# Performance work log

Measured on AMD Instinct MI355X. Metric: run time of the kernel, lower is better.

Reference implementation:

```python
import jax, jax.numpy as jnp
import numpy as np

B, N = 8192, 2048
_EPS = 1e-5


def setup_inputs() -> dict:
    key = jax.random.key(0)
    k1, k2, k3 = jax.random.split(key, 3)
    src = jax.random.normal(k1, (B, 3, N), dtype=jnp.float32)
    src_corr = jax.random.normal(k2, (B, 3, N), dtype=jnp.float32)
    weights = jax.random.uniform(k3, (B, N), dtype=jnp.float32)
    return {"src": src, "src_corr": src_corr, "weights": weights}


def reference(src, src_corr, weights):
    # src, src_corr: (B, 3, N); weights: (B, N)
    a = jnp.swapaxes(src, -1, -2)        # (B, N, 3)
    b = jnp.swapaxes(src_corr, -1, -2)   # (B, N, 3)
    w = weights[..., None]               # (B, N, 1)
    wn = w / (jnp.sum(w, axis=1, keepdims=True) + _EPS)
    centroid_a = jnp.sum(a * wn, axis=1)  # (B, 3)
    centroid_b = jnp.sum(b * wn, axis=1)  # (B, 3)
    a_c = a - centroid_a[:, None, :]
    b_c = b - centroid_b[:, None, :]
    # cov = a_c^T @ (b_c * wn) -> (B, 3, 3)
    cov = jnp.einsum('bnd,bne->bde', a_c, b_c * wn)
    u, s, vh = jnp.linalg.svd(cov, full_matrices=False)
    v = jnp.swapaxes(vh, -1, -2)
    ut = jnp.swapaxes(u, -1, -2)
    rot_pos = v @ ut
    v_neg = v.at[:, :, 2].multiply(-1.0)  # flip last column of v
    rot_neg = v_neg @ ut
    rot = jnp.where(jnp.linalg.det(rot_pos)[:, None, None] > 0, rot_pos, rot_neg)
    translation = centroid_b - jnp.einsum('bij,bj->bi', rot, centroid_a)  # (B, 3)
    return rot, translation
```

## Files before the change

kernel.cpp:

```cpp
#include <hip/hip_runtime.h>
#include <math.h>


constexpr int kB = 8192;
constexpr int kN = 2048;
constexpr float kEps = 1e-5f;

__global__ __launch_bounds__(256) void wproc_kernel(
    const float* __restrict__ src,
    const float* __restrict__ src_corr,
    const float* __restrict__ weights,
    float* __restrict__ out)
{
    const int b = blockIdx.x;
    const float* wrow = weights + (size_t)b * kN;
    const float* arow = src + (size_t)b * 3 * kN;
    const float* brow = src_corr + (size_t)b * 3 * kN;

    float acc[16];
#pragma unroll
    for (int i = 0; i < 16; ++i) acc[i] = 0.f;

    const float4* w4  = reinterpret_cast<const float4*>(wrow);
    const float4* ax4 = reinterpret_cast<const float4*>(arow);
    const float4* ay4 = reinterpret_cast<const float4*>(arow + kN);
    const float4* az4 = reinterpret_cast<const float4*>(arow + 2 * kN);
    const float4* bx4 = reinterpret_cast<const float4*>(brow);
    const float4* by4 = reinterpret_cast<const float4*>(brow + kN);
    const float4* bz4 = reinterpret_cast<const float4*>(brow + 2 * kN);

    for (int i = threadIdx.x; i < kN / 4; i += blockDim.x) {
        float4 w  = w4[i];
        float4 ax = ax4[i], ay = ay4[i], az = az4[i];
        float4 bx = bx4[i], by = by4[i], bz = bz4[i];
        float wc[4]  = {w.x,  w.y,  w.z,  w.w};
        float axc[4] = {ax.x, ax.y, ax.z, ax.w};
        float ayc[4] = {ay.x, ay.y, ay.z, ay.w};
        float azc[4] = {az.x, az.y, az.z, az.w};
        float bxc[4] = {bx.x, bx.y, bx.z, bx.w};
        float byc[4] = {by.x, by.y, by.z, by.w};
        float bzc[4] = {bz.x, bz.y, bz.z, bz.w};
#pragma unroll
        for (int c = 0; c < 4; ++c) {
            float ww  = wc[c];
            float wax = ww * axc[c], way = ww * ayc[c], waz = ww * azc[c];
            float bxx = bxc[c], byy = byc[c], bzz = bzc[c];
            acc[0]  += ww;
            acc[1]  += wax;       acc[2]  += way;       acc[3]  += waz;
            acc[4]  += ww * bxx;  acc[5]  += ww * byy;  acc[6]  += ww * bzz;
            acc[7]  += wax * bxx; acc[8]  += wax * byy; acc[9]  += wax * bzz;
            acc[10] += way * bxx; acc[11] += way * byy; acc[12] += way * bzz;
            acc[13] += waz * bxx; acc[14] += waz * byy; acc[15] += waz * bzz;
        }
    }

#pragma unroll
    for (int i = 0; i < 16; ++i) {
        float v = acc[i];
        for (int off = 32; off > 0; off >>= 1)
            v += __shfl_down(v, off, 64);
        acc[i] = v;
    }

    __shared__ float red[4][16];
    const int lane = threadIdx.x & 63;
    const int wid  = threadIdx.x >> 6;
    if (lane == 0) {
#pragma unroll
        for (int i = 0; i < 16; ++i) red[wid][i] = acc[i];
    }
    __syncthreads();
    if (threadIdx.x != 0) return;

    float t[16];
#pragma unroll
    for (int i = 0; i < 16; ++i)
        t[i] = red[0][i] + red[1][i] + red[2][i] + red[3][i];

    const float W   = t[0];
    const float inv = 1.f / (W + kEps);
    const float S   = W * inv;
    float ca[3], cb[3];
#pragma unroll
    for (int d = 0; d < 3; ++d) { ca[d] = t[1 + d] * inv; cb[d] = t[4 + d] * inv; }

    float M[3][3];
    const float f2 = 2.f - S;
#pragma unroll
    for (int d = 0; d < 3; ++d)
#pragma unroll
        for (int e = 0; e < 3; ++e)
            M[d][e] = t[7 + 3 * d + e] * inv - ca[d] * cb[e] * f2;

    const float T  = M[0][0] + M[1][1] + M[2][2];
    const float cx = M[1][2] - M[2][1];
    const float cy = M[2][0] - M[0][2];
    const float cz = M[0][1] - M[1][0];
    float Nm[4][4];
    Nm[0][0] = T;
    Nm[0][1] = Nm[1][0] = cx;
    Nm[0][2] = Nm[2][0] = cy;
    Nm[0][3] = Nm[3][0] = cz;
    Nm[1][1] = 2.f * M[0][0] - T;
    Nm[2][2] = 2.f * M[1][1] - T;
    Nm[3][3] = 2.f * M[2][2] - T;
    Nm[1][2] = Nm[2][1] = M[0][1] + M[1][0];
    Nm[1][3] = Nm[3][1] = M[0][2] + M[2][0];
    Nm[2][3] = Nm[3][2] = M[1][2] + M[2][1];

    float Vv[4][4] = {{1,0,0,0},{0,1,0,0},{0,0,1,0},{0,0,0,1}};
    const int pp[6] = {0,0,0,1,1,2};
    const int qq[6] = {1,2,3,2,3,3};
    for (int sweep = 0; sweep < 6; ++sweep) {
        for (int r = 0; r < 6; ++r) {
            const int p = pp[r], q = qq[r];
            const float apq = Nm[p][q];
            if (fabsf(apq) < 1e-12f) continue;
            const float tau = (Nm[q][q] - Nm[p][p]) / (2.f * apq);
            const float tt  = copysignf(1.f, tau) / (fabsf(tau) + sqrtf(1.f + tau * tau));
            const float c   = 1.f / sqrtf(1.f + tt * tt);
            const float s   = tt * c;
            const float app = Nm[p][p], aqq = Nm[q][q];
            Nm[p][p] = app - tt * apq;
            Nm[q][q] = aqq + tt * apq;
            Nm[p][q] = Nm[q][p] = 0.f;
#pragma unroll
            for (int k = 0; k < 4; ++k) {
                if (k == p || k == q) continue;
                const float akp = Nm[k][p], akq = Nm[k][q];
                Nm[k][p] = Nm[p][k] = c * akp - s * akq;
                Nm[k][q] = Nm[q][k] = s * akp + c * akq;
            }
#pragma unroll
            for (int k = 0; k < 4; ++k) {
                const float vkp = Vv[k][p], vkq = Vv[k][q];
                Vv[k][p] = c * vkp - s * vkq;
                Vv[k][q] = s * vkp + c * vkq;
            }
        }
    }

    int jm = 0;
    for (int j = 1; j < 4; ++j) if (Nm[j][j] > Nm[jm][jm]) jm = j;
    float qw = Vv[0][jm], qx = Vv[1][jm], qy = Vv[2][jm], qz = Vv[3][jm];
    const float nq = 1.f / sqrtf(qw * qw + qx * qx + qy * qy + qz * qz);
    qw *= nq; qx *= nq; qy *= nq; qz *= nq;

    float R[3][3];
    R[0][0] = 1.f - 2.f * (qy * qy + qz * qz);
    R[0][1] = 2.f * (qx * qy - qw * qz);
    R[0][2] = 2.f * (qx * qz + qw * qy);
    R[1][0] = 2.f * (qx * qy + qw * qz);
    R[1][1] = 1.f - 2.f * (qx * qx + qz * qz);
    R[1][2] = 2.f * (qy * qz - qw * qx);
    R[2][0] = 2.f * (qx * qz - qw * qy);
    R[2][1] = 2.f * (qy * qz + qw * qx);
    R[2][2] = 1.f - 2.f * (qx * qx + qy * qy);

    float* ro = out + (size_t)b * 9;
#pragma unroll
    for (int i = 0; i < 3; ++i)
#pragma unroll
        for (int j = 0; j < 3; ++j)
            ro[3 * i + j] = R[i][j];

    float* to = out + (size_t)kB * 9 + (size_t)b * 3;
#pragma unroll
    for (int i = 0; i < 3; ++i)
        to[i] = cb[i] - (R[i][0] * ca[0] + R[i][1] * ca[1] + R[i][2] * ca[2]);
}

extern "C" void kernel_launch(void* const* d_in, const int* in_sizes, int n_in,
                              void* d_out, int out_size, void* d_ws, size_t ws_size,
                              hipStream_t stream) {
    const float* src      = (const float*)d_in[0];
    const float* src_corr = (const float*)d_in[1];
    const float* weights  = (const float*)d_in[2];
    float* out = (float*)d_out;
    wproc_kernel<<<kB, 256, 0, stream>>>(src, src_corr, weights, out);
}
```

Measured before the change: 452.2 us.

## Split reduction and eigen-solve into two kernels with per-thread batched solve

Result: no change. 456.3 us (+0.9%).

```diff
diff --git a/kernel.cpp b/kernel.cpp
--- a/kernel.cpp
+++ b/kernel.cpp
@@ -6,45 +6,41 @@
 constexpr int kN = 2048;
 constexpr float kEps = 1e-5f;
 
-__global__ __launch_bounds__(256) void wproc_kernel(
+__global__ __launch_bounds__(512) void wproc_reduce(
     const float* __restrict__ src,
     const float* __restrict__ src_corr,
     const float* __restrict__ weights,
-    float* __restrict__ out)
+    float* __restrict__ ws)
 {
     const int b = blockIdx.x;
-    const float* wrow = weights + (size_t)b * kN;
+    const int tid = threadIdx.x;
     const float* arow = src + (size_t)b * 3 * kN;
     const float* brow = src_corr + (size_t)b * 3 * kN;
 
+    const float4 w  = reinterpret_cast<const float4*>(weights + (size_t)b * kN)[tid];
+    const float4 ax = reinterpret_cast<const float4*>(arow)[tid];
+    const float4 ay = reinterpret_cast<const float4*>(arow + kN)[tid];
+    const float4 az = reinterpret_cast<const float4*>(arow + 2 * kN)[tid];
+    const float4 bx = reinterpret_cast<const float4*>(brow)[tid];
+    const float4 by = reinterpret_cast<const float4*>(brow + kN)[tid];
+    const float4 bz = reinterpret_cast<const float4*>(brow + 2 * kN)[tid];
+
     float acc[16];
+    {
+        const float wc[4]  = {w.x,  w.y,  w.z,  w.w};
+        const float axc[4] = {ax.x, ax.y, ax.z, ax.w};
+        const float ayc[4] = {ay.x, ay.y, ay.z, ay.w};
+        const float azc[4] = {az.x, az.y, az.z, az.w};
+        const float bxc[4] = {bx.x, bx.y, bx.z, bx.w};
+        const float byc[4] = {by.x, by.y, by.z, by.w};
+        const float bzc[4] = {bz.x, bz.y, bz.z, bz.w};
 #pragma unroll
-    for (int i = 0; i < 16; ++i) acc[i] = 0.f;
-
-    const float4* w4  = reinterpret_cast<const float4*>(wrow);
-    const float4* ax4 = reinterpret_cast<const float4*>(arow);
-    const float4* ay4 = reinterpret_cast<const float4*>(arow + kN);
-    const float4* az4 = reinterpret_cast<const float4*>(arow + 2 * kN);
-    const float4* bx4 = reinterpret_cast<const float4*>(brow);
-    const float4* by4 = reinterpret_cast<const float4*>(brow + kN);
-    const float4* bz4 = reinterpret_cast<const float4*>(brow + 2 * kN);
-
-    for (int i = threadIdx.x; i < kN / 4; i += blockDim.x) {
-        float4 w  = w4[i];
-        float4 ax = ax4[i], ay = ay4[i], az = az4[i];
-        float4 bx = bx4[i], by = by4[i], bz = bz4[i];
-        float wc[4]  = {w.x,  w.y,  w.z,  w.w};
-        float axc[4] = {ax.x, ax.y, ax.z, ax.w};
-        float ayc[4] = {ay.x, ay.y, ay.z, ay.w};
-        float azc[4] = {az.x, az.y, az.z, az.w};
-        float bxc[4] = {bx.x, bx.y, bx.z, bx.w};
-        float byc[4] = {by.x, by.y, by.z, by.w};
-        float bzc[4] = {bz.x, bz.y, bz.z, bz.w};
+        for (int i = 0; i < 16; ++i) acc[i] = 0.f;
 #pragma unroll
         for (int c = 0; c < 4; ++c) {
-            float ww  = wc[c];
-            float wax = ww * axc[c], way = ww * ayc[c], waz = ww * azc[c];
-            float bxx = bxc[c], byy = byc[c], bzz = bzc[c];
+            const float ww  = wc[c];
+            const float wax = ww * axc[c], way = ww * ayc[c], waz = ww * azc[c];
+            const float bxx = bxc[c], byy = byc[c], bzz = bzc[c];
             acc[0]  += ww;
             acc[1]  += wax;       acc[2]  += way;       acc[3]  += waz;
             acc[4]  += ww * bxx;  acc[5]  += ww * byy;  acc[6]  += ww * bzz;
@@ -57,25 +53,41 @@
 #pragma unroll
     for (int i = 0; i < 16; ++i) {
         float v = acc[i];
+#pragma unroll
         for (int off = 32; off > 0; off >>= 1)
             v += __shfl_down(v, off, 64);
         acc[i] = v;
     }
 
-    __shared__ float red[4][16];
-    const int lane = threadIdx.x & 63;
-    const int wid  = threadIdx.x >> 6;
+    __shared__ float red[8][16];
+    const int lane = tid & 63;
+    const int wid  = tid >> 6;
     if (lane == 0) {
 #pragma unroll
         for (int i = 0; i < 16; ++i) red[wid][i] = acc[i];
     }
     __syncthreads();
-    if (threadIdx.x != 0) return;
+    if (tid < 16) {
+        float s = 0.f;
+#pragma unroll
+        for (int k = 0; k < 8; ++k) s += red[k][tid];
+        ws[(size_t)b * 16 + tid] = s;
+    }
+}
+
+__global__ __launch_bounds__(256) void wproc_solve(
+    const float* __restrict__ ws,
+    float* __restrict__ out)
+{
+    const int b = blockIdx.x * blockDim.x + threadIdx.x;
+    if (b >= kB) return;
 
     float t[16];
 #pragma unroll
-    for (int i = 0; i < 16; ++i)
-        t[i] = red[0][i] + red[1][i] + red[2][i] + red[3][i];
+    for (int i = 0; i < 4; ++i) {
+        const float4 v = reinterpret_cast<const float4*>(ws + (size_t)b * 16)[i];
+        t[4 * i] = v.x; t[4 * i + 1] = v.y; t[4 * i + 2] = v.z; t[4 * i + 3] = v.w;
+    }
 
     const float W   = t[0];
     const float inv = 1.f / (W + kEps);
@@ -141,6 +153,7 @@
     }
 
     int jm = 0;
+#pragma unroll
     for (int j = 1; j < 4; ++j) if (Nm[j][j] > Nm[jm][jm]) jm = j;
     float qw = Vv[0][jm], qx = Vv[1][jm], qy = Vv[2][jm], qz = Vv[3][jm];
     const float nq = 1.f / sqrtf(qw * qw + qx * qx + qy * qy + qz * qz);
@@ -177,5 +190,7 @@
     const float* src_corr = (const float*)d_in[1];
     const float* weights  = (const float*)d_in[2];
     float* out = (float*)d_out;
-    wproc_kernel<<<kB, 256, 0, stream>>>(src, src_corr, weights, out);
+    float* ws  = (float*)d_ws;
+    wproc_reduce<<<kB, 512, 0, stream>>>(src, src_corr, weights, ws);
+    wproc_solve<<<(kB + 255) / 256, 256, 0, stream>>>(ws, out);
 }
```
